# Performance work log

Measured on AMD Instinct MI355X. Metric: run time of the kernel, lower is better.

## Reference

```python
import jax, jax.numpy as jnp
import numpy as np

N = 8000   # nodes
E = 32000  # edges
B = 64     # graphs in batch
V = 5000   # vocab
D = 200    # embed dim; 20 tokens/node * 200 = 4000 = conv1 in_dim
T = 20


def setup_inputs() -> dict:
    key = jax.random.key(0)
    ks = jax.random.split(key, 12)
    return {
        "x": jax.random.randint(ks[0], (N, T), 0, V),
        "edge_index": jax.random.randint(ks[1], (2, E), 0, N),
        "batch": jnp.sort(jax.random.randint(ks[2], (N,), 0, B)),
        "emb": jax.random.normal(ks[3], (V, D), jnp.float32) * 0.02,
        "W1": jax.random.normal(ks[4], (4000, 6000), jnp.float32) * 0.01,
        "b1": jnp.zeros((6000,), jnp.float32),
        "W2": jax.random.normal(ks[5], (6000, 6000), jnp.float32) * 0.01,
        "b2": jnp.zeros((6000,), jnp.float32),
        "Wl1": jax.random.normal(ks[6], (6000, 3000), jnp.float32) * 0.01,
        "bl1": jnp.zeros((3000,), jnp.float32),
        "Wl2": jax.random.normal(ks[7], (3000, 4), jnp.float32) * 0.01,
        "bl2": jnp.zeros((4,), jnp.float32),
    }


def gcn_conv(h, W, b, src, dst, n):
    """PyG GCNConv: x' = D^-1/2 (A+I) D^-1/2 (x W) + b; src/dst include self-loops."""
    h = h @ W  # [n, out]
    deg = jax.ops.segment_sum(jnp.ones(dst.shape[0], h.dtype), dst, num_segments=n)
    dinv = jnp.where(deg > 0, jax.lax.rsqrt(deg), 0.0)
    norm = dinv[src] * dinv[dst]  # [E+n]
    agg = jax.ops.segment_sum(h[src] * norm[:, None], dst, num_segments=n)
    return agg + b


def reference(x, edge_index, batch, emb, W1, b1, W2, b2, Wl1, bl1, Wl2, bl2):
    n = x.shape[0]
    h = emb[x].reshape(n, -1)  # [N, 4000]
    loops = jnp.arange(n)
    src = jnp.concatenate([edge_index[0], loops])
    dst = jnp.concatenate([edge_index[1], loops])
    h = jax.nn.leaky_relu(gcn_conv(h, W1, b1, src, dst, n))  # dropout: identity in eval
    h = jax.nn.leaky_relu(gcn_conv(h, W2, b2, src, dst, n))
    g = jax.ops.segment_max(h, batch, num_segments=B)  # global_max_pool -> [B, 6000]
    g = jax.nn.leaky_relu(g @ Wl1 + bl1)
    return jax.nn.leaky_relu(g @ Wl2 + bl2)  # [B, 4]
```

## Files before the change

### kernel.cpp

```cpp
#include <hip/hip_runtime.h>
#include <hip/hip_bf16.h>

#define Nn 8000
#define Ee 32000
#define Bb 64
#define Dembed 200
#define Ttok 20
#define Mp 8192
#define K1 4096
#define K2 6144
#define L1p 3072
#define LCHUNK 256
#define NCH 24

#define GBM 256
#define GBN 256
#define GBK 64
#define ABUF (GBM * GBK)
#define BUFE (2 * ABUF)

#define LRELU(v) ((v) > 0.f ? (v) : 0.01f * (v))

typedef __attribute__((ext_vector_type(4))) float f32x4;
typedef __attribute__((ext_vector_type(8))) short s16x8;

#define GLL16(gp, lp) __builtin_amdgcn_global_load_lds( \
    (const __attribute__((address_space(1))) void*)(gp), \
    (__attribute__((address_space(3))) void*)(lp), 16, 0, 0)

__device__ __forceinline__ float b2f(short s) {
    union { unsigned u; float f; } c;
    c.u = ((unsigned)(unsigned short)s) << 16;
    return c.f;
}
__device__ __forceinline__ short f2b(float f) {
    __hip_bfloat16 h = __float2bfloat16(f);
    return __builtin_bit_cast(short, h);
}

__global__ __launch_bounds__(256)
void k_gather(const int* __restrict__ x, const float* __restrict__ emb,
              short* __restrict__ h0, int Wp)
{
    const int i = blockIdx.x;
    __shared__ int tok[Ttok];
    if (threadIdx.x < Ttok) tok[threadIdx.x] = x[i * Ttok + threadIdx.x];
    __syncthreads();
    for (int c = threadIdx.x; c < Wp; c += 256) {
        float v = 0.f;
        if (c < Ttok * Dembed) {
            int t = c / Dembed;
            int d = c - t * Dembed;
            v = emb[(long)tok[t] * Dembed + d];
        }
        h0[(long)i * Wp + c] = f2b(v);
    }
}

__global__ void k_deg(const int* __restrict__ dst, int* __restrict__ indeg) {
    int e = blockIdx.x * 256 + threadIdx.x;
    if (e < Ee) atomicAdd(&indeg[dst[e]], 1);
}

__global__ void k_dinv(const int* __restrict__ indeg, float* __restrict__ dinv) {
    int i = blockIdx.x * 256 + threadIdx.x;
    if (i < Nn) dinv[i] = rsqrtf((float)indeg[i] + 1.0f);
}

__global__ __launch_bounds__(1024)
void k_scan(const int* __restrict__ indeg, int* __restrict__ rowptr, int n)
{
    __shared__ int sums[1024];
    const int t = threadIdx.x;
    const int base = t * 8;
    int loc[8];
    int s = 0;
#pragma unroll
    for (int j = 0; j < 8; ++j) {
        int v = (base + j < n) ? indeg[base + j] : 0;
        loc[j] = s; s += v;
    }
    sums[t] = s;
    __syncthreads();
    for (int off = 1; off < 1024; off <<= 1) {
        int v = sums[t];
        int add = (t >= off) ? sums[t - off] : 0;
        __syncthreads();
        sums[t] = v + add;
        __syncthreads();
    }
    const int prev = (t == 0) ? 0 : sums[t - 1];
#pragma unroll
    for (int j = 0; j < 8; ++j)
        if (base + j < n) rowptr[base + j] = prev + loc[j];
    if (t == 1023) rowptr[n] = sums[1023];
}

__global__ void k_fill(const int* __restrict__ src, const int* __restrict__ dst,
                       const int* __restrict__ rowptr, int* __restrict__ fillc,
                       int* __restrict__ csr) {
    int e = blockIdx.x * 256 + threadIdx.x;
    if (e < Ee) {
        int d = dst[e];
        int pos = rowptr[d] + atomicAdd(&fillc[d], 1);
        csr[pos] = src[e];
    }
}

template<int NG>
__global__ __launch_bounds__(256)
void k_agg(const short* __restrict__ Hin, short* __restrict__ Hout,
           const float* __restrict__ dinv, const int* __restrict__ rowptr,
           const int* __restrict__ csr, int Wp)
{
    const int i = blockIdx.x;
    const int tid = threadIdx.x;
    const float di = dinv[i];
    const float wself = di * di;
    const long rowi = (long)i * Wp;
    float acc[NG * 8];
#pragma unroll
    for (int gI = 0; gI < NG; ++gI) {
        s16x8 v = *(const s16x8*)(Hin + rowi + gI * 2048 + tid * 8);
#pragma unroll
        for (int j = 0; j < 8; ++j) acc[gI * 8 + j] = wself * b2f(v[j]);
    }
    const int e0 = rowptr[i], e1 = rowptr[i + 1];
    for (int e = e0; e < e1; ++e) {
        const int s = csr[e];
        const float w = dinv[s] * di;
        const long rows = (long)s * Wp;
#pragma unroll
        for (int gI = 0; gI < NG; ++gI) {
            s16x8 v = *(const s16x8*)(Hin + rows + gI * 2048 + tid * 8);
#pragma unroll
            for (int j = 0; j < 8; ++j) acc[gI * 8 + j] += w * b2f(v[j]);
        }
    }
#pragma unroll
    for (int gI = 0; gI < NG; ++gI) {
        s16x8 o;
#pragma unroll
        for (int j = 0; j < 8; ++j) o[j] = f2b(acc[gI * 8 + j]);
        *(s16x8*)(Hout + rowi + gI * 2048 + tid * 8) = o;
    }
}

__global__ void k_transpose(const float* __restrict__ In, short* __restrict__ Out,
                            int K, int N, int Kp, int Np)
{
    __shared__ float tile[32][33];
    const int k0 = blockIdx.x * 32;
    const int n0 = blockIdx.y * 32;
    const int tx = threadIdx.x, ty = threadIdx.y;
#pragma unroll
    for (int yy = ty; yy < 32; yy += 8) {
        int k = k0 + yy, n = n0 + tx;
        tile[yy][tx] = (k < K && n < N) ? In[(long)k * N + n] : 0.f;
    }
    __syncthreads();
#pragma unroll
    for (int yy = ty; yy < 32; yy += 8) {
        int n = n0 + yy, k = k0 + tx;
        if (n < Np && k < Kp) Out[(long)n * Kp + k] = f2b(tile[tx][yy]);
    }
}

__global__ __launch_bounds__(512, 2)
void k_gemm8p(const short* __restrict__ A, const short* __restrict__ Bt,
              short* __restrict__ C, const float* __restrict__ bias,
              int K, int Np, int Nreal, int nbx)
{
    __shared__ short lds[2 * BUFE];

    const int tid  = threadIdx.x;
    const int lane = tid & 63;
    const int wid  = tid >> 6;
    const int wm   = wid >> 2;
    const int wn   = wid & 3;

    const int cpx = (int)gridDim.x >> 3;
    const int bid = (int)blockIdx.x;
    const int swz = (bid & 7) * cpx + (bid >> 3);
    const int bx = swz % nbx;
    const int by = swz / nbx;

    const int rq = tid >> 3;
    const int kq = ((tid & 7) << 3) ^ ((rq & 7) << 3);
    const short* Abase = A  + ((long)by * GBM + rq) * K + kq;
    const short* Bbase = Bt + ((long)bx * GBN + rq) * K + kq;

#define ST2(bb, t2, base, ldoff, c0_, c1_) do { \
    const short* g0_ = (base) + (long)((c0_) * 64) * K + (long)(t2) * GBK; \
    const short* g1_ = (base) + (long)((c1_) * 64) * K + (long)(t2) * GBK; \
    GLL16(g0_, lds + (bb) * BUFE + (ldoff) + (c0_) * 4096 + tid * 8); \
    GLL16(g1_, lds + (bb) * BUFE + (ldoff) + (c1_) * 4096 + tid * 8); \
  } while (0)

    const int fr  = lane & 15;
    const int kb8 = (lane >> 4) << 3;
    const int xm  = (fr & 7) << 3;
    const int ck0 = kb8 ^ xm;
    const int ck1 = (32 + kb8) ^ xm;
    const int aoff = (wm * 128 + fr) * 64;
    const int boff = ABUF + (wn * 64 + fr) * 64;

    f32x4 acc[8][4] = {};
    s16x8 av[4], bv[4];

    const int NT = K >> 6;

    ST2(0, 0, Bbase, ABUF, 0, 1);
    ST2(0, 0, Bbase, ABUF, 2, 3);
    ST2(0, 0, Abase, 0,    0, 2);
    ST2(0, 0, Abase, 0,    1, 3);
    asm volatile("s_waitcnt vmcnt(2)" ::: "memory");
    __builtin_amdgcn_s_barrier();

    int buf = 0;
    for (int t = 0; t < NT; ++t) {
        const short* lb = lds + buf * BUFE;
        const int nb = buf ^ 1;
        const bool pf = (t + 1 < NT);

#pragma unroll
        for (int n = 0; n < 4; ++n) bv[n] = *(const s16x8*)(lb + boff + n * 1024 + ck0);
#pragma unroll
        for (int m = 0; m < 4; ++m) av[m] = *(const s16x8*)(lb + aoff + m * 1024 + ck0);
        if (pf) {
            ST2(nb, t + 1, Bbase, ABUF, 0, 1);
            asm volatile("s_waitcnt vmcnt(2)" ::: "memory");
        } else {
            asm volatile("s_waitcnt vmcnt(0)" ::: "memory");
        }
        __builtin_amdgcn_s_barrier();
        __builtin_amdgcn_s_setprio(1);
#pragma unroll
        for (int m = 0; m < 4; ++m)
#pragma unroll
            for (int n = 0; n < 4; ++n)
                acc[m][n] = __builtin_amdgcn_mfma_f32_16x16x32_bf16(av[m], bv[n], acc[m][n], 0, 0, 0);
        __builtin_amdgcn_s_setprio(0);
        __builtin_amdgcn_s_barrier();

#pragma unroll
        for (int m = 0; m < 4; ++m) av[m] = *(const s16x8*)(lb + aoff + (4 + m) * 1024 + ck0);
        if (pf) ST2(nb, t + 1, Bbase, ABUF, 2, 3);
        __builtin_amdgcn_s_barrier();
        __builtin_amdgcn_s_setprio(1);
#pragma unroll
        for (int m = 0; m < 4; ++m)
#pragma unroll
            for (int n = 0; n < 4; ++n)
                acc[4 + m][n] = __builtin_amdgcn_mfma_f32_16x16x32_bf16(av[m], bv[n], acc[4 + m][n], 0, 0, 0);
        __builtin_amdgcn_s_setprio(0);
        __builtin_amdgcn_s_barrier();

#pragma unroll
        for (int n = 0; n < 4; ++n) bv[n] = *(const s16x8*)(lb + boff + n * 1024 + ck1);
#pragma unroll
        for (int m = 0; m < 4; ++m) av[m] = *(const s16x8*)(lb + aoff + (4 + m) * 1024 + ck1);
        if (pf) ST2(nb, t + 1, Abase, 0, 0, 2);
        __builtin_amdgcn_s_barrier();
        __builtin_amdgcn_s_setprio(1);
#pragma unroll
        for (int m = 0; m < 4; ++m)
#pragma unroll
            for (int n = 0; n < 4; ++n)
                acc[4 + m][n] = __builtin_amdgcn_mfma_f32_16x16x32_bf16(av[m], bv[n], acc[4 + m][n], 0, 0, 0);
        __builtin_amdgcn_s_setprio(0);
        __builtin_amdgcn_s_barrier();

#pragma unroll
        for (int m = 0; m < 4; ++m) av[m] = *(const s16x8*)(lb + aoff + m * 1024 + ck1);
        if (pf) ST2(nb, t + 1, Abase, 0, 1, 3);
        __builtin_amdgcn_s_barrier();
        __builtin_amdgcn_s_setprio(1);
#pragma unroll
        for (int m = 0; m < 4; ++m)
#pragma unroll
            for (int n = 0; n < 4; ++n)
                acc[m][n] = __builtin_amdgcn_mfma_f32_16x16x32_bf16(av[m], bv[n], acc[m][n], 0, 0, 0);
        __builtin_amdgcn_s_setprio(0);
        if (pf) asm volatile("s_waitcnt vmcnt(2)" ::: "memory");
        __builtin_amdgcn_s_barrier();

        buf = nb;
    }

    const int rr = (lane >> 4) << 2;
#pragma unroll
    for (int n = 0; n < 4; ++n) {
        const long col = (long)bx * GBN + wn * 64 + n * 16 + fr;
        const float bvv = (col < Nreal) ? bias[col] : 0.f;
#pragma unroll
        for (int m = 0; m < 8; ++m) {
#pragma unroll
            for (int j = 0; j < 4; ++j) {
                const long row = (long)by * GBM + wm * 128 + m * 16 + rr + j;
                float v = acc[m][n][j] + bvv;
                v = LRELU(v);
                C[row * Np + col] = f2b(v);
            }
        }
    }
#undef ST2
}

__global__ void k_bptr(const int* __restrict__ batch, int* __restrict__ bptr) {
    int i = blockIdx.x * 256 + threadIdx.x;
    if (i >= Nn) return;
    int b = batch[i];
    int pb = (i == 0) ? -1 : batch[i - 1];
    for (int bb = pb + 1; bb <= b; ++bb) bptr[bb] = i;
    if (i == Nn - 1)
        for (int bb = b + 1; bb <= Bb; ++bb) bptr[bb] = Nn;
}

__global__ __launch_bounds__(256)
void k_pool(const short* __restrict__ h2, const int* __restrict__ bptr,
            float* __restrict__ g, int Wp) {
    int col = blockIdx.x * 256 + threadIdx.x;
    int b = blockIdx.y;
    float m = -INFINITY;
    int i0 = bptr[b], i1 = bptr[b + 1];
    for (int i = i0; i < i1; ++i)
        m = fmaxf(m, b2f(h2[(long)i * Wp + col]));
    g[b * Wp + col] = m;
}

__global__ __launch_bounds__(256)
void k_lin1_part(const float* __restrict__ g, const float* __restrict__ Wl1,
                 float* __restrict__ part) {
    __shared__ float gs[64][65];
    __shared__ float Ws[64][64];
    const int tid = threadIdx.x;
    const int jc = blockIdx.x * 64;
    const int k0 = blockIdx.y * LCHUNK;
    const int k1 = min(6000, k0 + LCHUNK);
    const int r = tid & 63;
    const int jb = (tid >> 6) * 16;
    float acc[16] = {};
    for (int kc = k0; kc < k1; kc += 64) {
#pragma unroll
        for (int p = 0; p < 16; ++p) {
            int el = p * 256 + tid;
            int rr = el >> 6, kk = el & 63;
            gs[rr][kk] = (kc + kk < k1) ? g[rr * K2 + kc + kk] : 0.f;
            Ws[rr][kk] = (kc + rr < k1 && jc + kk < 3000)
                         ? Wl1[(long)(kc + rr) * 3000 + jc + kk] : 0.f;
        }
        __syncthreads();
#pragma unroll
        for (int k = 0; k < 64; ++k) {
            float a = gs[r][k];
#pragma unroll
            for (int jj = 0; jj < 16; ++jj)
                acc[jj] += a * Ws[k][jb + jj];
        }
        __syncthreads();
    }
    float* prow = part + ((long)blockIdx.y * 64 + r) * L1p + jc + jb;
#pragma unroll
    for (int jj = 0; jj < 16; ++jj) prow[jj] = acc[jj];
}

__global__ __launch_bounds__(256)
void k_lin1_red(const float* __restrict__ part, const float* __restrict__ bl1,
                float* __restrict__ g1) {
    int idx = blockIdx.x * 256 + threadIdx.x;
    if (idx >= 64 * 3000) return;
    int r = idx / 3000;
    int c = idx - r * 3000;
    float s = bl1[c];
#pragma unroll
    for (int p = 0; p < NCH; ++p)
        s += part[((long)p * 64 + r) * L1p + c];
    g1[r * L1p + c] = LRELU(s);
}

__global__ __launch_bounds__(256)
void k_lin2(const float* __restrict__ g1, const float* __restrict__ Wl2,
            const float* __restrict__ bl2, float* __restrict__ out) {
    const int r = blockIdx.x;
    const int tid = threadIdx.x;
    float a0 = 0, a1 = 0, a2 = 0, a3 = 0;
    for (int k = tid; k < 3000; k += 256) {
        float gv = g1[r * L1p + k];
        const float* w = Wl2 + (long)k * 4;
        a0 += gv * w[0]; a1 += gv * w[1]; a2 += gv * w[2]; a3 += gv * w[3];
    }
    __shared__ float red[256][4];
    red[tid][0] = a0; red[tid][1] = a1; red[tid][2] = a2; red[tid][3] = a3;
    __syncthreads();
    for (int s = 128; s > 0; s >>= 1) {
        if (tid < s) {
            red[tid][0] += red[tid + s][0]; red[tid][1] += red[tid + s][1];
            red[tid][2] += red[tid + s][2]; red[tid][3] += red[tid + s][3];
        }
        __syncthreads();
    }
    if (tid < 4) {
        float v = red[0][tid] + bl2[tid];
        out[r * 4 + tid] = LRELU(v);
    }
}

extern "C" void kernel_launch(void* const* d_in, const int* in_sizes, int n_in,
                              void* d_out, int out_size, void* d_ws, size_t ws_size,
                              hipStream_t stream)
{
    const int*   x     = (const int*)d_in[0];
    const int*   ei    = (const int*)d_in[1];
    const int*   batch = (const int*)d_in[2];
    const float* emb   = (const float*)d_in[3];
    const float* W1    = (const float*)d_in[4];
    const float* b1    = (const float*)d_in[5];
    const float* W2    = (const float*)d_in[6];
    const float* b2    = (const float*)d_in[7];
    const float* Wl1   = (const float*)d_in[8];
    const float* bl1   = (const float*)d_in[9];
    const float* Wl2   = (const float*)d_in[10];
    const float* bl2   = (const float*)d_in[11];
    float* out = (float*)d_out;

    const int* esrc = ei;
    const int* edst = ei + Ee;

    const size_t MiB = 1ull << 20;
    char* W = (char*)d_ws;
    short* h0b  = (short*)(W + 0);
    short* Ah0b = (short*)(W + 64 * MiB);
    short* W2t  = (short*)(W + 96 * MiB);
    short* W1t  = (short*)(W + 128 * MiB);
    short* h1b  = (short*)(W + 176 * MiB);
    short* Ah1b = (short*)(W + 0);
    short* h2b  = h1b;
    float* part = (float*)(W + 0);
    char* S = W + 272 * MiB;
    int*   indeg  = (int*)(S);
    float* dinv   = (float*)(S + 32 * 1024);
    int*   rowptr = (int*)(S + 64 * 1024);
    int*   fillc  = (int*)(S + 96 * 1024);
    int*   csr    = (int*)(S + 128 * 1024);
    int*   bptr   = (int*)(S + 256 * 1024);
    float* g      = (float*)(S + 320 * 1024);
    float* g1     = (float*)(S + 320 * 1024 + 2 * MiB);

    hipMemsetAsync(indeg, 0, Nn * sizeof(int), stream);
    hipMemsetAsync(fillc, 0, Nn * sizeof(int), stream);

    k_gather<<<Nn, 256, 0, stream>>>(x, emb, h0b, K1);
    k_deg<<<(Ee + 255) / 256, 256, 0, stream>>>(edst, indeg);
    k_dinv<<<(Nn + 255) / 256, 256, 0, stream>>>(indeg, dinv);
    k_scan<<<1, 1024, 0, stream>>>(indeg, rowptr, Nn);
    k_fill<<<(Ee + 255) / 256, 256, 0, stream>>>(esrc, edst, rowptr, fillc, csr);

    const int nbx = K2 / GBN;
    const int nwg = nbx * (Mp / GBM);

    k_agg<2><<<Nn, 256, 0, stream>>>(h0b, Ah0b, dinv, rowptr, csr, K1);
    k_transpose<<<dim3(K1 / 32, K2 / 32), dim3(32, 8), 0, stream>>>(W1, W1t, 4000, 6000, K1, K2);
    k_gemm8p<<<nwg, 512, 0, stream>>>(Ah0b, W1t, h1b, b1, K1, K2, 6000, nbx);

    k_transpose<<<dim3(K2 / 32, K2 / 32), dim3(32, 8), 0, stream>>>(W2, W2t, 6000, 6000, K2, K2);
    k_agg<3><<<Nn, 256, 0, stream>>>(h1b, Ah1b, dinv, rowptr, csr, K2);
    k_gemm8p<<<nwg, 512, 0, stream>>>(Ah1b, W2t, h2b, b2, K2, K2, 6000, nbx);

    k_bptr<<<(Nn + 255) / 256, 256, 0, stream>>>(batch, bptr);
    k_pool<<<dim3(K2 / 256, Bb), 256, 0, stream>>>(h2b, bptr, g, K2);
    k_lin1_part<<<dim3(L1p / 64, NCH), 256, 0, stream>>>(g, Wl1, part);
    k_lin1_red<<<(64 * 3000 + 255) / 256, 256, 0, stream>>>(part, bl1, g1);
    k_lin2<<<Bb, 256, 0, stream>>>(g1, Wl2, bl2, out);
}
```

Before: 1.410 ms.

## Deepen GEMM prefetch to two stages ahead and vectorize max-pool loads

The GEMM main loop now issues the first B half-tile for step t+2 into the buffer being consumed, keeping more global loads in flight, and rebalances the vmcnt waits to match. The goal is to hide more global memory latency behind the MFMA phases. It risks a race if the current buffer is overwritten before every wave has finished reading it. Separately, the max-pool kernel now loads 8 bf16 values per thread with one vector load and launches 8x fewer blocks.

```diff
diff --git a/kernel.cpp b/kernel.cpp
--- a/kernel.cpp
+++ b/kernel.cpp
@@ -214,25 +214,22 @@
     ST2(0, 0, Bbase, ABUF, 2, 3);
     ST2(0, 0, Abase, 0,    0, 2);
     ST2(0, 0, Abase, 0,    1, 3);
-    asm volatile("s_waitcnt vmcnt(2)" ::: "memory");
+    ST2(1, 1, Bbase, ABUF, 0, 1);
+    asm volatile("s_waitcnt vmcnt(4)" ::: "memory");
     __builtin_amdgcn_s_barrier();
 
     int buf = 0;
     for (int t = 0; t < NT; ++t) {
         const short* lb = lds + buf * BUFE;
         const int nb = buf ^ 1;
-        const bool pf = (t + 1 < NT);
+        const bool pf1 = (t + 1 < NT);
+        const bool pf2 = (t + 2 < NT);
 
 #pragma unroll
         for (int n = 0; n < 4; ++n) bv[n] = *(const s16x8*)(lb + boff + n * 1024 + ck0);
 #pragma unroll
         for (int m = 0; m < 4; ++m) av[m] = *(const s16x8*)(lb + aoff + m * 1024 + ck0);
-        if (pf) {
-            ST2(nb, t + 1, Bbase, ABUF, 0, 1);
-            asm volatile("s_waitcnt vmcnt(2)" ::: "memory");
-        } else {
-            asm volatile("s_waitcnt vmcnt(0)" ::: "memory");
-        }
+        if (pf1) ST2(nb, t + 1, Bbase, ABUF, 2, 3);
         __builtin_amdgcn_s_barrier();
         __builtin_amdgcn_s_setprio(1);
 #pragma unroll
@@ -241,11 +238,13 @@
             for (int n = 0; n < 4; ++n)
                 acc[m][n] = __builtin_amdgcn_mfma_f32_16x16x32_bf16(av[m], bv[n], acc[m][n], 0, 0, 0);
         __builtin_amdgcn_s_setprio(0);
+        if (pf1) asm volatile("s_waitcnt vmcnt(4)" ::: "memory");
+        else     asm volatile("s_waitcnt vmcnt(0)" ::: "memory");
         __builtin_amdgcn_s_barrier();
 
 #pragma unroll
         for (int m = 0; m < 4; ++m) av[m] = *(const s16x8*)(lb + aoff + (4 + m) * 1024 + ck0);
-        if (pf) ST2(nb, t + 1, Bbase, ABUF, 2, 3);
+        if (pf1) ST2(nb, t + 1, Abase, 0, 0, 2);
         __builtin_amdgcn_s_barrier();
         __builtin_amdgcn_s_setprio(1);
 #pragma unroll
@@ -260,7 +259,7 @@
         for (int n = 0; n < 4; ++n) bv[n] = *(const s16x8*)(lb + boff + n * 1024 + ck1);
 #pragma unroll
         for (int m = 0; m < 4; ++m) av[m] = *(const s16x8*)(lb + aoff + (4 + m) * 1024 + ck1);
-        if (pf) ST2(nb, t + 1, Abase, 0, 0, 2);
+        if (pf1) ST2(nb, t + 1, Abase, 0, 1, 3);
         __builtin_amdgcn_s_barrier();
         __builtin_amdgcn_s_setprio(1);
 #pragma unroll
@@ -273,7 +272,7 @@
 
 #pragma unroll
         for (int m = 0; m < 4; ++m) av[m] = *(const s16x8*)(lb + aoff + m * 1024 + ck1);
-        if (pf) ST2(nb, t + 1, Abase, 0, 1, 3);
+        if (pf2) ST2(buf, t + 2, Bbase, ABUF, 0, 1);
         __builtin_amdgcn_s_barrier();
         __builtin_amdgcn_s_setprio(1);
 #pragma unroll
@@ -282,7 +281,8 @@
             for (int n = 0; n < 4; ++n)
                 acc[m][n] = __builtin_amdgcn_mfma_f32_16x16x32_bf16(av[m], bv[n], acc[m][n], 0, 0, 0);
         __builtin_amdgcn_s_setprio(0);
-        if (pf) asm volatile("s_waitcnt vmcnt(2)" ::: "memory");
+        if (pf2)      asm volatile("s_waitcnt vmcnt(4)" ::: "memory");
+        else if (pf1) asm volatile("s_waitcnt vmcnt(2)" ::: "memory");
         __builtin_amdgcn_s_barrier();
 
         buf = nb;
@@ -320,13 +320,20 @@
 __global__ __launch_bounds__(256)
 void k_pool(const short* __restrict__ h2, const int* __restrict__ bptr,
             float* __restrict__ g, int Wp) {
-    int col = blockIdx.x * 256 + threadIdx.x;
-    int b = blockIdx.y;
-    float m = -INFINITY;
-    int i0 = bptr[b], i1 = bptr[b + 1];
-    for (int i = i0; i < i1; ++i)
-        m = fmaxf(m, b2f(h2[(long)i * Wp + col]));
-    g[b * Wp + col] = m;
+    const int c8 = blockIdx.x * 256 + threadIdx.x;
+    const int b = blockIdx.y;
+    const short* base = h2 + (long)c8 * 8;
+    float mx[8];
+#pragma unroll
+    for (int j = 0; j < 8; ++j) mx[j] = -INFINITY;
+    const int i0 = bptr[b], i1 = bptr[b + 1];
+    for (int i = i0; i < i1; ++i) {
+        s16x8 v = *(const s16x8*)(base + (long)i * Wp);
+#pragma unroll
+        for (int j = 0; j < 8; ++j) mx[j] = fmaxf(mx[j], b2f(v[j]));
+    }
+#pragma unroll
+    for (int j = 0; j < 8; ++j) g[(long)b * Wp + c8 * 8 + j] = mx[j];
 }
 
 __global__ __launch_bounds__(256)
@@ -468,7 +475,7 @@
     k_gemm8p<<<nwg, 512, 0, stream>>>(Ah1b, W2t, h2b, b2, K2, K2, 6000, nbx);
 
     k_bptr<<<(Nn + 255) / 256, 256, 0, stream>>>(batch, bptr);
-    k_pool<<<dim3(K2 / 256, Bb), 256, 0, stream>>>(h2b, bptr, g, K2);
+    k_pool<<<dim3(K2 / 2048, Bb), 256, 0, stream>>>(h2b, bptr, g, K2);
     k_lin1_part<<<dim3(L1p / 64, NCH), 256, 0, stream>>>(g, Wl1, part);
     k_lin1_red<<<(64 * 3000 + 255) / 256, 256, 0, stream>>>(part, bl1, g1);
     k_lin2<<<Bb, 256, 0, stream>>>(g1, Wl2, bl2, out);
```

New measurement: 1.393 ms. About the same (-1.2%).
